# Kernel tuning notes

Measured on AMD Instinct MI355X. Metric: run time of the kernel, lower is better.

## Reference

```python
import jax, jax.numpy as jnp
import numpy as np

EPS_BN = 1e-5
EPS_NORM = 1e-12
NUM_HEADS = 8


def _bn_relu(x):
    # BatchNorm2d in training mode with fresh params (gamma=1, beta=0), then ReLU.
    m = x.mean((0, 2, 3), keepdims=True)
    v = x.var((0, 2, 3), keepdims=True)  # biased variance, as PyTorch uses for normalization
    return jax.nn.relu((x - m) * jax.lax.rsqrt(v + EPS_BN))


def _conv3(x, w, groups=1):
    # 3x3 conv, stride 1, padding 1 (NCHW / OIHW)
    return jax.lax.conv_general_dilated(
        x, w, (1, 1), ((1, 1), (1, 1)),
        dimension_numbers=('NCHW', 'OIHW', 'NCHW'),
        feature_group_count=groups)


def _encoder(x, w1, w2, w3):
    # Conv1x1 -> BN -> ReLU -> Conv k2 s2 -> BN -> ReLU -> Conv1x1 -> BN -> ReLU
    x = _bn_relu(jnp.einsum('bihw,oi->bohw', x, w1))
    b, c, h, w = x.shape
    # k=2,s=2 conv as a reshape + einsum (non-overlapping 2x2 patches)
    x = _bn_relu(jnp.einsum('bchpwq,ocpq->bohw', x.reshape(b, c, h // 2, 2, w // 2, 2), w2))
    return _bn_relu(jnp.einsum('bihw,oi->bohw', x, w3))


def _decoder(x, w1, w2, w3):
    # ConvT1x1 -> BN -> ReLU -> ConvT k2 s2 -> BN -> ReLU -> ConvT1x1 -> BN -> ReLU
    x = _bn_relu(jnp.einsum('bihw,io->bohw', x, w1))
    # ConvTranspose k=2,s=2: each input pixel expands to a 2x2 block
    y = jnp.einsum('bihw,iopq->bohpwq', x, w2)
    b, o, h, p, w, q = y.shape
    x = _bn_relu(y.reshape(b, o, h * p, w * q))
    return _bn_relu(jnp.einsum('bihw,io->bohw', x, w3))


def _l2norm(x):
    # F.normalize(dim=-1) with eps=1e-12
    return x / jnp.maximum(jnp.linalg.norm(x, axis=-1, keepdims=True), EPS_NORM)


def setup_inputs() -> dict:
    key = jax.random.key(0)
    ks = jax.random.split(key, 13)
    B, C, H, W = 8, 256, 64, 64
    d = C // 4  # attention dim after self.divide

    def rn(k, shape, s=0.1):
        return jax.random.normal(k, shape, jnp.float32) * s

    return {
        'x': jax.random.normal(ks[0], (B, C, H, W), jnp.float32),
        'y': jax.random.normal(ks[1], (B, C, H, W), jnp.float32),
        'temperature': jnp.ones((NUM_HEADS, 1, 1), jnp.float32),
        'enc_w1': rn(ks[2], (d // 2, C)),
        'enc_w2': rn(ks[3], (d // 2, d // 2, 2, 2)),
        'enc_w3': rn(ks[4], (d, d // 2)),
        'kv_w': rn(ks[5], (2 * d, d)),
        'kv_dw_w': rn(ks[6], (2 * d, 1, 3, 3)),
        'q_w': rn(ks[7], (d, d)),
        'q_dw_w': rn(ks[8], (d, d, 3, 3)),
        'proj_w': rn(ks[9], (d, d)),
        'dec_w1': rn(ks[10], (d, 2 * d)),
        'dec_w2': rn(ks[11], (2 * d, 2 * d, 2, 2)),
        'dec_w3': rn(ks[12], (2 * d, 4 * d)),
    }


def reference(x, y, temperature, enc_w1, enc_w2, enc_w3, kv_w, kv_dw_w,
              q_w, q_dw_w, proj_w, dec_w1, dec_w2, dec_w3):
    # Shared freshly-built encoder applied to both x and y (same weights,
    # BN batch stats computed per call).
    x = _encoder(x, enc_w1, enc_w2, enc_w3)
    y = _encoder(y, enc_w1, enc_w2, enc_w3)
    b, c, h, w = x.shape  # c = 64, h = w = 32

    kv = _conv3(jnp.einsum('bihw,oi->bohw', x, kv_w), kv_dw_w, groups=2 * c)
    k, v = jnp.split(kv, 2, axis=1)
    q = _conv3(jnp.einsum('bihw,oi->bohw', y, q_w), q_dw_w)  # regular 3x3 conv

    ch = c // NUM_HEADS
    heads = lambda t: t.reshape(b, NUM_HEADS, ch, h * w)  # b head c (h w)
    q, k, v = heads(q), heads(k), heads(v)
    q = _l2norm(q)
    k = _l2norm(k)
    temp = temperature[None]  # [1, head, 1, 1]

    # Spatial attention: [b, head, hw, hw]
    attn_s = jax.nn.softmax(jnp.einsum('bhcn,bhcm->bhnm', q, k) * temp, axis=-1)
    out_s = jnp.einsum('bhcn,bhnm->bhcm', v, attn_s).reshape(b, c, h, w)
    out_s = jnp.einsum('bihw,oi->bohw', out_s, proj_w)

    # Channel attention: [b, head, c, c]
    attn_c = jax.nn.softmax(jnp.einsum('bhcn,bhdn->bhcd', q, k) * temp, axis=-1)
    out_c = jnp.einsum('bhcd,bhdn->bhcn', attn_c, v).reshape(b, c, h, w)
    out_c = jnp.einsum('bihw,oi->bohw', out_c, proj_w)

    return _decoder(out_s + out_c, dec_w1, dec_w2, dec_w3)
```

## Files before the change

### kernel.cpp

```cpp
#include <hip/hip_runtime.h>
#include <hip/hip_bf16.h>

#define EPS_BN 1e-5f

template<int OT, bool HASBN, bool HASSTATS>
__global__ __launch_bounds__(256) void conv1x1_kernel(
    const float* __restrict__ in0, const float* __restrict__ in1,
    const float* __restrict__ w, float* __restrict__ out,
    const float* __restrict__ stIn, float* __restrict__ stOut,
    int I, int O, int P, int wio, int zsplit, float invN)
{
  __shared__ float wl[2048];
  __shared__ float bnm[256], bnr[256];
  int tid = threadIdx.x;
  int o0 = blockIdx.y*OT;
  int z  = blockIdx.z;
  int t  = (z >= zsplit) ? 1 : 0;
  int b  = t ? (z - zsplit) : z;
  const float* in = t ? in1 : in0;

  for(int idx=tid; idx<I*OT; idx+=256){
    int i = idx/OT, j = idx - i*OT;
    wl[idx] = wio ? w[(size_t)i*O + o0 + j] : w[(size_t)(o0+j)*I + i];
  }
  if(HASBN){
    for(int i=tid; i<I; i+=256){
      float s  = stIn[((size_t)t*I + i)*2];
      float s2 = stIn[((size_t)t*I + i)*2+1];
      float m  = s*invN;
      bnm[i] = m;
      bnr[i] = rsqrtf(s2*invN - m*m + EPS_BN);
    }
  }
  __syncthreads();

  int p4 = blockIdx.x*256 + tid;
  const float4* inb = (const float4*)(in + (size_t)b*I*P) + p4;
  int P4 = P >> 2;

  float acc[OT][4];
#pragma unroll
  for(int j=0;j<OT;j++){ acc[j][0]=acc[j][1]=acc[j][2]=acc[j][3]=0.f; }

  float4 vb[8];
  for(int i0=0;i0<I;i0+=8){
#pragma unroll
    for(int u=0;u<8;u++) vb[u] = inb[(size_t)(i0+u)*P4];
#pragma unroll
    for(int u=0;u<8;u++){
      float4 v = vb[u];
      if(HASBN){
        float m = bnm[i0+u], r = bnr[i0+u];
        v.x = fmaxf((v.x-m)*r, 0.f); v.y = fmaxf((v.y-m)*r, 0.f);
        v.z = fmaxf((v.z-m)*r, 0.f); v.w = fmaxf((v.w-m)*r, 0.f);
      }
      const float* wr = &wl[(i0+u)*OT];
#pragma unroll
      for(int j=0;j<OT;j++){
        float wv = wr[j];
        acc[j][0] = fmaf(wv, v.x, acc[j][0]);
        acc[j][1] = fmaf(wv, v.y, acc[j][1]);
        acc[j][2] = fmaf(wv, v.z, acc[j][2]);
        acc[j][3] = fmaf(wv, v.w, acc[j][3]);
      }
    }
  }

  float4* ob = (float4*)(out + ((size_t)z*O + o0)*P) + p4;
#pragma unroll
  for(int j=0;j<OT;j++){
    float4 vv = {acc[j][0], acc[j][1], acc[j][2], acc[j][3]};
    ob[(size_t)j*P4] = vv;
  }

  if(HASSTATS){
#pragma unroll
    for(int j=0;j<OT;j++){
      float s  = acc[j][0]+acc[j][1]+acc[j][2]+acc[j][3];
      float s2 = acc[j][0]*acc[j][0]+acc[j][1]*acc[j][1]
               + acc[j][2]*acc[j][2]+acc[j][3]*acc[j][3];
      for(int off=32; off>0; off>>=1){
        s  += __shfl_down(s,  off, 64);
        s2 += __shfl_down(s2, off, 64);
      }
      if((tid & 63)==0){
        atomicAdd(&stOut[((size_t)t*O + o0 + j)*2],   s);
        atomicAdd(&stOut[((size_t)t*O + o0 + j)*2+1], s2);
      }
    }
  }
}

template<int OT, bool HASBN, bool HASSTATS>
__global__ __launch_bounds__(256) void conv1x1_small(
    const float* __restrict__ in0, const float* __restrict__ in1,
    const float* __restrict__ w, float* __restrict__ out,
    const float* __restrict__ stIn, float* __restrict__ stOut,
    int I, int O, int wio, int zsplit, float invN)
{
  __shared__ float wl[512];
  __shared__ float bnm[128], bnr[128];
  int tid = threadIdx.x;
  int z  = blockIdx.z;
  int t  = (z >= zsplit) ? 1 : 0;
  int b  = t ? (z - zsplit) : z;
  const float* in = t ? in1 : in0;
  int W2 = 2*OT;

  for(int idx=tid; idx<I*W2; idx+=256){
    int i = idx/W2, slot = idx - i*W2;
    int oabs = blockIdx.y*W2 + slot;
    wl[idx] = wio ? w[(size_t)i*O + oabs] : w[(size_t)oabs*I + i];
  }
  if(HASBN){
    for(int i=tid; i<I; i+=256){
      float s  = stIn[((size_t)t*I + i)*2];
      float s2 = stIn[((size_t)t*I + i)*2+1];
      float m  = s*invN;
      bnm[i] = m;
      bnr[i] = rsqrtf(s2*invN - m*m + EPS_BN);
    }
  }
  __syncthreads();

  int p4 = blockIdx.x*128 + (tid & 127);
  int os = tid >> 7;
  const float4* inb = (const float4*)(in + (size_t)b*I*1024) + p4;

  float acc[OT][4];
#pragma unroll
  for(int j=0;j<OT;j++){ acc[j][0]=acc[j][1]=acc[j][2]=acc[j][3]=0.f; }

  float4 vb[8];
  for(int i0=0;i0<I;i0+=8){
#pragma unroll
    for(int u=0;u<8;u++) vb[u] = inb[(size_t)(i0+u)*256];
#pragma unroll
    for(int u=0;u<8;u++){
      float4 v = vb[u];
      if(HASBN){
        float m = bnm[i0+u], r = bnr[i0+u];
        v.x = fmaxf((v.x-m)*r, 0.f); v.y = fmaxf((v.y-m)*r, 0.f);
        v.z = fmaxf((v.z-m)*r, 0.f); v.w = fmaxf((v.w-m)*r, 0.f);
      }
      const float* wr = &wl[(i0+u)*W2 + os*OT];
#pragma unroll
      for(int j=0;j<OT;j++){
        float wv = wr[j];
        acc[j][0] = fmaf(wv, v.x, acc[j][0]);
        acc[j][1] = fmaf(wv, v.y, acc[j][1]);
        acc[j][2] = fmaf(wv, v.z, acc[j][2]);
        acc[j][3] = fmaf(wv, v.w, acc[j][3]);
      }
    }
  }

  int obase = blockIdx.y*W2 + os*OT;
  float4* ob = (float4*)(out + ((size_t)z*O + obase)*1024) + p4;
#pragma unroll
  for(int j=0;j<OT;j++){
    float4 vv = {acc[j][0], acc[j][1], acc[j][2], acc[j][3]};
    ob[(size_t)j*256] = vv;
  }

  if(HASSTATS){
#pragma unroll
    for(int j=0;j<OT;j++){
      float s  = acc[j][0]+acc[j][1]+acc[j][2]+acc[j][3];
      float s2 = acc[j][0]*acc[j][0]+acc[j][1]*acc[j][1]
               + acc[j][2]*acc[j][2]+acc[j][3]*acc[j][3];
      for(int off=32; off>0; off>>=1){
        s  += __shfl_down(s,  off, 64);
        s2 += __shfl_down(s2, off, 64);
      }
      if((tid & 63)==0){
        atomicAdd(&stOut[((size_t)t*O + obase + j)*2],   s);
        atomicAdd(&stOut[((size_t)t*O + obase + j)*2+1], s2);
      }
    }
  }
}

__global__ __launch_bounds__(256) void conv2x2s2_bn_kernel(
    const float* __restrict__ in, const float* __restrict__ w,
    float* __restrict__ out, const float* __restrict__ stIn,
    float* __restrict__ stOut, float invN)
{
  __shared__ float wl[512];
  __shared__ float bnm[32], bnr[32];
  int tid = threadIdx.x;
  int o0 = blockIdx.x*4;
  int rq = blockIdx.y;
  int z  = blockIdx.z;
  int t  = z >> 3;

  for(int idx=tid; idx<512; idx+=256){
    int osub = idx>>7, ch=(idx>>2)&31, pq=idx&3;
    wl[idx] = w[(((size_t)(o0+osub)*32 + ch)*4) + pq];
  }
  if(tid < 32){
    float s  = stIn[((size_t)t*32 + tid)*2];
    float s2 = stIn[((size_t)t*32 + tid)*2+1];
    float m  = s*invN;
    bnm[tid] = m;
    bnr[tid] = rsqrtf(s2*invN - m*m + EPS_BN);
  }
  __syncthreads();

  int os   = tid >> 6;
  int slot = tid & 63;
  int h    = rq*8 + (slot>>3);
  int wg   = slot & 7;
  int cb   = wg*8;
  const float* wbase = &wl[os*128];
  const float* inz = in + (size_t)z*32*4096;

  float acc[4] = {0,0,0,0};
  float4 c0,c1,c2,c3, n0_,n1_,n2_,n3_;
  c0 = *(const float4*)(inz + (size_t)0*4096 + (2*h)*64 + cb);
  c1 = *(const float4*)(inz + (size_t)0*4096 + (2*h)*64 + cb + 4);
  c2 = *(const float4*)(inz + (size_t)0*4096 + (2*h+1)*64 + cb);
  c3 = *(const float4*)(inz + (size_t)0*4096 + (2*h+1)*64 + cb + 4);
  for(int ch=0; ch<32; ch++){
    if(ch < 31){
      n0_ = *(const float4*)(inz + (size_t)(ch+1)*4096 + (2*h)*64 + cb);
      n1_ = *(const float4*)(inz + (size_t)(ch+1)*4096 + (2*h)*64 + cb + 4);
      n2_ = *(const float4*)(inz + (size_t)(ch+1)*4096 + (2*h+1)*64 + cb);
      n3_ = *(const float4*)(inz + (size_t)(ch+1)*4096 + (2*h+1)*64 + cb + 4);
    }
    float m = bnm[ch], r = bnr[ch];
    float t0[8] = {c0.x,c0.y,c0.z,c0.w,c1.x,c1.y,c1.z,c1.w};
    float t1[8] = {c2.x,c2.y,c2.z,c2.w,c3.x,c3.y,c3.z,c3.w};
#pragma unroll
    for(int e=0;e<8;e++){
      t0[e] = fmaxf((t0[e]-m)*r, 0.f);
      t1[e] = fmaxf((t1[e]-m)*r, 0.f);
    }
    const float* wp = wbase + ch*4;
#pragma unroll
    for(int k=0;k<4;k++){
      acc[k] = fmaf(wp[0], t0[2*k],   acc[k]);
      acc[k] = fmaf(wp[1], t0[2*k+1], acc[k]);
      acc[k] = fmaf(wp[2], t1[2*k],   acc[k]);
      acc[k] = fmaf(wp[3], t1[2*k+1], acc[k]);
    }
    c0=n0_; c1=n1_; c2=n2_; c3=n3_;
  }

  float4 vv = {acc[0],acc[1],acc[2],acc[3]};
  *(float4*)(out + ((size_t)z*32 + o0+os)*1024 + h*32 + wg*4) = vv;

  float s  = acc[0]+acc[1]+acc[2]+acc[3];
  float s2 = acc[0]*acc[0]+acc[1]*acc[1]+acc[2]*acc[2]+acc[3]*acc[3];
  for(int off=32; off>0; off>>=1){
    s  += __shfl_down(s,  off, 64);
    s2 += __shfl_down(s2, off, 64);
  }
  if((tid & 63)==0){
    atomicAdd(&stOut[((size_t)t*32 + o0 + os)*2],   s);
    atomicAdd(&stOut[((size_t)t*32 + o0 + os)*2+1], s2);
  }
}

__global__ __launch_bounds__(256) void upsample2x2_bn_kernel(
    const float* __restrict__ in, const float* __restrict__ w,
    float* __restrict__ out, const float* __restrict__ stIn,
    float* __restrict__ stOut, float invN)
{
  __shared__ float wl[1024];
  __shared__ float bnm[128], bnr[128];
  int tid = threadIdx.x;
  int o0 = blockIdx.x*2;
  int b  = blockIdx.y;

  for(int idx=tid; idx<1024; idx+=256){
    int pq = idx & 3, r = idx >> 2;
    int i = r >> 1, j = r & 1;
    wl[idx] = w[((size_t)i*128 + o0+j)*4 + pq];
  }
  if(tid < 128){
    float s  = stIn[(size_t)tid*2];
    float s2 = stIn[(size_t)tid*2+1];
    float m  = s*invN;
    bnm[tid] = m;
    bnr[tid] = rsqrtf(s2*invN - m*m + EPS_BN);
  }
  __syncthreads();

  int h  = tid >> 3;
  int wg = tid & 7;
  int w0 = wg*4;

  float acc[2][16];
#pragma unroll
  for(int j=0;j<2;j++) for(int e=0;e<16;e++) acc[j][e]=0.f;

  float4 vb4[8];
  for(int i0=0;i0<128;i0+=8){
#pragma unroll
    for(int u=0;u<8;u++)
      vb4[u] = *(const float4*)(in + (((size_t)b*128+i0+u)*1024) + h*32 + w0);
#pragma unroll
    for(int u=0;u<8;u++){
      int i = i0+u;
      float4 v = vb4[u];
      float m = bnm[i], r = bnr[i];
      float vk[4] = {fmaxf((v.x-m)*r,0.f), fmaxf((v.y-m)*r,0.f),
                     fmaxf((v.z-m)*r,0.f), fmaxf((v.w-m)*r,0.f)};
#pragma unroll
      for(int j=0;j<2;j++){
        const float* wj = &wl[(i*2+j)*4];
#pragma unroll
        for(int pq=0;pq<4;pq++){
#pragma unroll
          for(int k=0;k<4;k++)
            acc[j][pq*4+k] = fmaf(wj[pq], vk[k], acc[j][pq*4+k]);
        }
      }
    }
  }

#pragma unroll
  for(int j=0;j<2;j++){
    float* ob = out + ((size_t)b*128 + o0+j)*4096;
#pragma unroll
    for(int p=0;p<2;p++){
      float4 A = {acc[j][(p*2+0)*4+0], acc[j][(p*2+1)*4+0],
                  acc[j][(p*2+0)*4+1], acc[j][(p*2+1)*4+1]};
      float4 B = {acc[j][(p*2+0)*4+2], acc[j][(p*2+1)*4+2],
                  acc[j][(p*2+0)*4+3], acc[j][(p*2+1)*4+3]};
      *(float4*)(ob + (2*h+p)*64 + 2*w0)     = A;
      *(float4*)(ob + (2*h+p)*64 + 2*w0 + 4) = B;
    }
  }

#pragma unroll
  for(int j=0;j<2;j++){
    float s=0.f, s2=0.f;
#pragma unroll
    for(int e=0;e<16;e++){ s += acc[j][e]; s2 += acc[j][e]*acc[j][e]; }
    for(int off=32; off>0; off>>=1){
      s  += __shfl_down(s,  off, 64);
      s2 += __shfl_down(s2, off, 64);
    }
    if((tid & 63)==0){
      atomicAdd(&stOut[((size_t)(o0+j))*2],   s);
      atomicAdd(&stOut[((size_t)(o0+j))*2+1], s2);
    }
  }
}

__global__ __launch_bounds__(256) void bn_final_kernel(
    float* __restrict__ x, const float* __restrict__ st, float invN)
{
  int idx4 = blockIdx.x*256 + threadIdx.x;
  int c = (idx4 >> 10) & 255;
  float s  = st[(size_t)c*2];
  float s2 = st[(size_t)c*2+1];
  float m  = s*invN;
  float r  = rsqrtf(s2*invN - m*m + EPS_BN);
  float4 v = ((float4*)x)[idx4];
  v.x = fmaxf((v.x-m)*r, 0.f); v.y = fmaxf((v.y-m)*r, 0.f);
  v.z = fmaxf((v.z-m)*r, 0.f); v.w = fmaxf((v.w-m)*r, 0.f);
  ((float4*)x)[idx4] = v;
}

__global__ __launch_bounds__(256) void dwconv3x3_kernel(
    const float* __restrict__ in, const float* __restrict__ w,
    float* __restrict__ out, int C)
{
  int c = blockIdx.x, b = blockIdx.y;
  int tid = threadIdx.x;
  __shared__ float wl[9];
  if(tid < 9) wl[tid] = w[c*9 + tid];
  __syncthreads();
  int h = tid >> 3, x4 = tid & 7;
  int c0 = x4*4;
  const float* base = in + ((size_t)b*C + c)*1024;
  float ax=0.f, ay=0.f, az=0.f, aw=0.f;
#pragma unroll
  for(int dr=0; dr<3; dr++){
    int r = h + dr - 1;
    if((unsigned)r >= 32u) continue;
    const float* row = base + r*32 + c0;
    float4 cc = *(const float4*)row;
    float l  = (x4>0) ? row[-1] : 0.f;
    float rr = (x4<7) ? row[4]  : 0.f;
    float w0=wl[dr*3], w1=wl[dr*3+1], w2=wl[dr*3+2];
    ax = fmaf(w0,l,   fmaf(w1,cc.x, fmaf(w2,cc.y, ax)));
    ay = fmaf(w0,cc.x,fmaf(w1,cc.y, fmaf(w2,cc.z, ay)));
    az = fmaf(w0,cc.y,fmaf(w1,cc.z, fmaf(w2,cc.w, az)));
    aw = fmaf(w0,cc.z,fmaf(w1,cc.w, fmaf(w2,rr,  aw)));
  }
  float4 vv = {ax,ay,az,aw};
  *(float4*)(out + ((size_t)b*C + c)*1024 + h*32 + c0) = vv;
}

__global__ __launch_bounds__(256) void conv3x3_kernel(
    const float* __restrict__ in, const float* __restrict__ w,
    float* __restrict__ out, int IC)
{
  int o = blockIdx.x, b = blockIdx.y;
  int tid = threadIdx.x;
  __shared__ float wl[576];
  for(int t=tid; t<IC*9; t+=256) wl[t] = w[(size_t)o*IC*9 + t];
  __syncthreads();
  int h = tid >> 3, x4 = tid & 7;
  int c0 = x4*4;
  const float* inb = in + (size_t)b*IC*1024;
  float ax=0.f, ay=0.f, az=0.f, aw=0.f;
#pragma unroll 2
  for(int i=0;i<IC;i++){
    const float* base = inb + (size_t)i*1024;
    const float* wp = &wl[i*9];
#pragma unroll
    for(int dr=0; dr<3; dr++){
      int r = h + dr - 1;
      if((unsigned)r >= 32u) continue;
      const float* row = base + r*32 + c0;
      float4 cc = *(const float4*)row;
      float l  = (x4>0) ? row[-1] : 0.f;
      float rr = (x4<7) ? row[4]  : 0.f;
      float w0=wp[dr*3], w1=wp[dr*3+1], w2=wp[dr*3+2];
      ax = fmaf(w0,l,   fmaf(w1,cc.x, fmaf(w2,cc.y, ax)));
      ay = fmaf(w0,cc.x,fmaf(w1,cc.y, fmaf(w2,cc.z, ay)));
      az = fmaf(w0,cc.y,fmaf(w1,cc.z, fmaf(w2,cc.w, az)));
      aw = fmaf(w0,cc.z,fmaf(w1,cc.w, fmaf(w2,rr,  aw)));
    }
  }
  float4 vv = {ax,ay,az,aw};
  *(float4*)(out + ((size_t)b*gridDim.x + o)*1024 + h*32 + c0) = vv;
}

__global__ __launch_bounds__(256) void norm_scale_kernel(
    const float* __restrict__ q, const float* __restrict__ kv,
    float* __restrict__ scl)
{
  int r = blockIdx.x;
  const float* p;
  if(r < 512){ int b=r>>6, c=r&63; p = q + ((size_t)b*64+c)*1024; }
  else { int rr=r-512; int b=rr>>6, c=rr&63; p = kv + ((size_t)b*128+c)*1024; }
  int tid = threadIdx.x;
  float4 v = ((const float4*)p)[tid];
  float s = v.x*v.x + v.y*v.y + v.z*v.z + v.w*v.w;
  __shared__ float ls[256];
  ls[tid]=s; __syncthreads();
  for(int st=128; st>0; st>>=1){ if(tid<st) ls[tid]+=ls[tid+st]; __syncthreads(); }
  if(tid==0) scl[r] = 1.f/fmaxf(sqrtf(ls[0]), 1e-12f);
}

__global__ __launch_bounds__(256) void attn_pass1(
    const float* __restrict__ q, const float* __restrict__ kv,
    const float* __restrict__ temp, const float* __restrict__ scl,
    float* __restrict__ den_out)
{
  int bx = blockIdx.x, hh = blockIdx.y, b = blockIdx.z;
  int nchunk = bx >> 2, mq = bx & 3;
  int tid = threadIdx.x;
  __shared__ __align__(16) float kl[256*12];
  const float* kb = kv + ((size_t)b*128 + hh*8)*1024 + mq*256;
  for(int t=tid;t<2048;t+=256){
    int c=t>>8, m=t&255;
    kl[m*12+c] = kb[(size_t)c*1024+m] * scl[512 + b*64 + hh*8 + c];
  }
  __syncthreads();
  int n = nchunk*256 + tid;
  const float* qp = q + ((size_t)b*64 + hh*8)*1024 + n;
  float th = temp[hh];
  float mxb = fabsf(th);
  float qr[8];
#pragma unroll
  for(int c=0;c<8;c++) qr[c] = qp[(size_t)c*1024] * scl[b*64+hh*8+c] * th;
  const float4* kl4 = (const float4*)kl;
  float den = 0.f, den2 = 0.f;
  for(int m=0;m<256;m+=2){
    float4 a  = kl4[m*3],     a2 = kl4[m*3+1];
    float4 bt = kl4[(m+1)*3], b2 = kl4[(m+1)*3+1];
    float s0 = qr[0]*a.x+qr[1]*a.y+qr[2]*a.z+qr[3]*a.w
             + qr[4]*a2.x+qr[5]*a2.y+qr[6]*a2.z+qr[7]*a2.w;
    float s1 = qr[0]*bt.x+qr[1]*bt.y+qr[2]*bt.z+qr[3]*bt.w
             + qr[4]*b2.x+qr[5]*b2.y+qr[6]*b2.z+qr[7]*b2.w;
    den  += __expf(s0 - mxb);
    den2 += __expf(s1 - mxb);
  }
  atomicAdd(&den_out[((size_t)(b*8+hh))*1024+n], den+den2);
}

__global__ __launch_bounds__(256) void attn_pass2(
    const float* __restrict__ q, const float* __restrict__ kv,
    const float* __restrict__ temp, const float* __restrict__ scl,
    const float* __restrict__ den, float* __restrict__ out)
{
  int bx = blockIdx.x, hh = blockIdx.y, b = blockIdx.z;
  int mchunk = bx >> 2, nq = bx & 3;
  int tid = threadIdx.x;
  __shared__ __align__(16) float ql[256*12];
  __shared__ __align__(16) float vl[256*12];
  __shared__ float idl[256];
  int bh = b*8+hh;
  int n0 = nq*256;
  const float* qb = q  + ((size_t)b*64 + hh*8)*1024 + n0;
  const float* vb = kv + ((size_t)b*128 + 64 + hh*8)*1024 + n0;
  for(int t=tid;t<2048;t+=256){
    int c=t>>8, n=t&255;
    ql[n*12+c] = qb[(size_t)c*1024+n] * scl[b*64+hh*8+c];
    vl[n*12+c] = vb[(size_t)c*1024+n];
  }
  idl[tid] = 1.f/den[(size_t)bh*1024 + n0 + tid];
  __syncthreads();
  int m = mchunk*256 + tid;
  const float* kb = kv + ((size_t)b*128 + hh*8)*1024 + m;
  float th = temp[hh];
  float mxb = fabsf(th);
  float kr[8];
#pragma unroll
  for(int c=0;c<8;c++) kr[c] = kb[(size_t)c*1024] * scl[512+b*64+hh*8+c] * th;
  float acc[8] = {0,0,0,0,0,0,0,0};
  const float4* ql4 = (const float4*)ql;
  const float4* vl4 = (const float4*)vl;
  for(int n=0;n<256;n+=2){
    float4 qa = ql4[n*3],     qa2 = ql4[n*3+1];
    float4 qc = ql4[(n+1)*3], qc2 = ql4[(n+1)*3+1];
    float s0 = kr[0]*qa.x+kr[1]*qa.y+kr[2]*qa.z+kr[3]*qa.w
             + kr[4]*qa2.x+kr[5]*qa2.y+kr[6]*qa2.z+kr[7]*qa2.w;
    float s1 = kr[0]*qc.x+kr[1]*qc.y+kr[2]*qc.z+kr[3]*qc.w
             + kr[4]*qc2.x+kr[5]*qc2.y+kr[6]*qc2.z+kr[7]*qc2.w;
    float p0 = __expf(s0 - mxb) * idl[n];
    float p1 = __expf(s1 - mxb) * idl[n+1];
    float4 va = vl4[n*3],     va2 = vl4[n*3+1];
    float4 vc = vl4[(n+1)*3], vc2 = vl4[(n+1)*3+1];
    acc[0]+=p0*va.x + p1*vc.x; acc[1]+=p0*va.y + p1*vc.y;
    acc[2]+=p0*va.z + p1*vc.z; acc[3]+=p0*va.w + p1*vc.w;
    acc[4]+=p0*va2.x + p1*vc2.x; acc[5]+=p0*va2.y + p1*vc2.y;
    acc[6]+=p0*va2.z + p1*vc2.z; acc[7]+=p0*va2.w + p1*vc2.w;
  }
  float* ob = out + ((size_t)b*64 + hh*8)*1024 + m;
#pragma unroll
  for(int c=0;c<8;c++) atomicAdd(&ob[(size_t)c*1024], acc[c]);
}

__global__ __launch_bounds__(256) void attn_channel(
    const float* __restrict__ q, const float* __restrict__ kv,
    const float* __restrict__ temp, const float* __restrict__ scl,
    float* out)
{
  int hh = blockIdx.x, b = blockIdx.y;
  __shared__ float kl[8192];
  const float* qb = q  + ((size_t)b*64 + hh*8)*1024;
  const float* kb = kv + ((size_t)b*128 + hh*8)*1024;
  const float* vb = kv + ((size_t)b*128 + 64 + hh*8)*1024;
  int tid = threadIdx.x;
  for(int t=tid;t<8192;t+=256) kl[t]=kb[t];
  __syncthreads();
  __shared__ float part[256];
  __shared__ float a[64];
  {
    int pair = tid >> 2, seg = tid & 3;
    int c = pair >> 3, d = pair & 7;
    const float* qrow = qb + (size_t)c*1024 + seg*256;
    const float* krow = kl + d*1024 + seg*256;
    float s = 0.f;
#pragma unroll 4
    for(int n=0;n<256;n++) s += qrow[n]*krow[n];
    part[tid] = s;
  }
  __syncthreads();
  if(tid < 64){
    int c = tid >> 3, d = tid & 7;
    float g = part[tid*4]+part[tid*4+1]+part[tid*4+2]+part[tid*4+3];
    part[tid] = g * scl[b*64+hh*8+c] * scl[512+b*64+hh*8+d] * temp[hh];
  }
  __syncthreads();
  if(tid < 8){
    float mx = -3.4e38f;
    for(int d=0;d<8;d++) mx = fmaxf(mx, part[tid*8+d]);
    float den = 0.f;
    float e[8];
    for(int d=0;d<8;d++){ e[d] = __expf(part[tid*8+d]-mx); den+=e[d]; }
    float inv = 1.f/den;
    for(int d=0;d<8;d++) a[tid*8+d] = e[d]*inv;
  }
  __syncthreads();
  float* ob = out + ((size_t)b*64 + hh*8)*1024;
  for(int n=tid;n<1024;n+=256){
    float vv[8];
#pragma unroll
    for(int d=0;d<8;d++) vv[d] = vb[(size_t)d*1024+n];
#pragma unroll
    for(int c=0;c<8;c++){
      float s = 0.f;
#pragma unroll
      for(int d=0;d<8;d++) s += a[c*8+d]*vv[d];
      ob[(size_t)c*1024+n] += s;
    }
  }
}

extern "C" void kernel_launch(void* const* d_in, const int* in_sizes, int n_in,
                              void* d_out, int out_size, void* d_ws, size_t ws_size,
                              hipStream_t stream)
{
  (void)in_sizes; (void)n_in; (void)out_size; (void)ws_size;
  const float* x      = (const float*)d_in[0];
  const float* y      = (const float*)d_in[1];
  const float* temp   = (const float*)d_in[2];
  const float* enc_w1 = (const float*)d_in[3];
  const float* enc_w2 = (const float*)d_in[4];
  const float* enc_w3 = (const float*)d_in[5];
  const float* kv_w   = (const float*)d_in[6];
  const float* kv_dw_w= (const float*)d_in[7];
  const float* q_w    = (const float*)d_in[8];
  const float* q_dw_w = (const float*)d_in[9];
  const float* proj_w = (const float*)d_in[10];
  const float* dec_w1 = (const float*)d_in[11];
  const float* dec_w2 = (const float*)d_in[12];
  const float* dec_w3 = (const float*)d_in[13];
  float* out = (float*)d_out;

  float* W   = (float*)d_ws;
  float* ST  = W;
  float* ST0 = ST;
  float* ST1 = ST + 128;
  float* ST2 = ST + 256;
  float* ST3 = ST + 512;
  float* ST4 = ST + 768;
  float* ST5 = ST + 1024;
  float* A    = W + 2048;
  float* E1   = A;
  float* KV1  = A;
  float* QPre = A + 1048576;
  float* ATTN = A;
  float* PROJ = A + 524288;
  float* D1   = A + 1048576;
  float* E2   = W + 2099200;
  float* E3   = W + 2623488;
  float* KV   = W + 3672064;
  float* Q    = W + 4720640;
  float* SCL  = W + 5244928;
  float* DEN  = W + 5245952;
  float* D2   = W + 2099200;

  const float inv32k = 1.f/32768.f, inv8k = 1.f/8192.f;

  hipMemsetAsync(ST, 0, 2048*sizeof(float), stream);
  hipMemsetAsync(DEN, 0, 65536*sizeof(float), stream);

  conv1x1_kernel<4,false,true><<<dim3(4,8,16),256,0,stream>>>(
      x, y, enc_w1, E1, nullptr, ST0, 256, 32, 4096, 0, 8, 0.f);
  conv2x2s2_bn_kernel<<<dim3(8,4,16),256,0,stream>>>(E1, enc_w2, E2, ST0, ST1, inv32k);
  conv1x1_small<1,true,true><<<dim3(2,32,16),256,0,stream>>>(
      E2, E2 + (size_t)8*32*1024, enc_w3, E3, ST1, ST2, 32, 64, 0, 8, inv8k);

  conv1x1_small<1,true,false><<<dim3(2,64,8),256,0,stream>>>(
      E3, E3, kv_w, KV1, ST2, nullptr, 64, 128, 0, 999, inv8k);
  dwconv3x3_kernel<<<dim3(128,8),256,0,stream>>>(KV1, kv_dw_w, KV, 128);
  conv1x1_small<1,true,false><<<dim3(2,32,8),256,0,stream>>>(
      E3 + (size_t)8*64*1024, E3, q_w, QPre, ST2 + 128, nullptr, 64, 64, 0, 999, inv8k);
  conv3x3_kernel<<<dim3(64,8),256,0,stream>>>(QPre, q_dw_w, Q, 64);

  hipMemsetAsync(ATTN, 0, 524288*sizeof(float), stream);

  norm_scale_kernel<<<1024,256,0,stream>>>(Q, KV, SCL);

  attn_pass1<<<dim3(16,8,8),256,0,stream>>>(Q, KV, temp, SCL, DEN);
  attn_pass2<<<dim3(16,8,8),256,0,stream>>>(Q, KV, temp, SCL, DEN, ATTN);
  attn_channel<<<dim3(8,8),256,0,stream>>>(Q, KV, temp, SCL, ATTN);

  conv1x1_small<1,false,false><<<dim3(2,32,8),256,0,stream>>>(
      ATTN, ATTN, proj_w, PROJ, nullptr, nullptr, 64, 64, 0, 999, 0.f);

  conv1x1_small<1,false,true><<<dim3(2,64,8),256,0,stream>>>(
      PROJ, PROJ, dec_w1, D1, nullptr, ST3, 64, 128, 1, 999, 0.f);
  upsample2x2_bn_kernel<<<dim3(64,8),256,0,stream>>>(D1, dec_w2, D2, ST3, ST4, inv8k);
  conv1x1_kernel<8,true,true><<<dim3(4,32,8),256,0,stream>>>(
      D2, D2, dec_w3, out, ST4, ST5, 128, 256, 4096, 1, 999, inv32k);
  bn_final_kernel<<<8192,256,0,stream>>>(out, ST5, inv32k);
}
```

Before: 589.7 us.

## Stage 1x1 conv inputs in double-buffered LDS and raise output tiling

The large 1x1 conv kernel now stages an 8-channel input slab in double-buffered shared memory. That slab is shared by 4 wavefronts, and each wavefront computes a different group of output channels. Input is therefore read once per block for all outputs instead of once per output tile, and weights are read as float4. The small 1x1 convs get a larger per-thread output count with fewer blocks, and compiler memory fences are added to keep the loads grouped. The cost is higher register and LDS use and fewer blocks in the grid, which may reduce occupancy.

```diff
diff --git a/kernel.cpp b/kernel.cpp
--- a/kernel.cpp
+++ b/kernel.cpp
@@ -3,25 +3,40 @@
 
 #define EPS_BN 1e-5f
 
+#define PIPE_FENCE() asm volatile("" ::: "memory")
+
 template<int OT, bool HASBN, bool HASSTATS>
-__global__ __launch_bounds__(256) void conv1x1_kernel(
+__global__ __launch_bounds__(256,2) void conv1x1_lds(
     const float* __restrict__ in0, const float* __restrict__ in1,
     const float* __restrict__ w, float* __restrict__ out,
     const float* __restrict__ stIn, float* __restrict__ stOut,
     int I, int O, int P, int wio, int zsplit, float invN)
 {
-  __shared__ float wl[2048];
+  constexpr int OB = 4*OT;
+  __shared__ __align__(16) float wl[8192];
+  __shared__ __align__(16) float4 il[2][8][64];
   __shared__ float bnm[256], bnr[256];
-  int tid = threadIdx.x;
-  int o0 = blockIdx.y*OT;
-  int z  = blockIdx.z;
-  int t  = (z >= zsplit) ? 1 : 0;
-  int b  = t ? (z - zsplit) : z;
+
+  int tid = threadIdx.x;
+  int c   = tid & 63;
+  int g   = tid >> 6;
+  int z = blockIdx.z;
+  int t = (z >= zsplit) ? 1 : 0;
+  int b = t ? (z - zsplit) : z;
   const float* in = t ? in1 : in0;
-
-  for(int idx=tid; idx<I*OT; idx+=256){
-    int i = idx/OT, j = idx - i*OT;
-    wl[idx] = wio ? w[(size_t)i*O + o0 + j] : w[(size_t)(o0+j)*I + i];
+  int o0 = blockIdx.y*OB;
+  int P4 = P >> 2;
+
+  if(wio){
+    for(int idx=tid; idx<I*OB; idx+=256){
+      int i = idx/OB, oo = idx - i*OB;
+      wl[idx] = w[(size_t)i*O + o0 + oo];
+    }
+  } else {
+    for(int idx=tid; idx<I*OB; idx+=256){
+      int oo = idx/I, i = idx - oo*I;
+      wl[i*OB + oo] = w[(size_t)(o0+oo)*I + i];
+    }
   }
   if(HASBN){
     for(int i=tid; i<I; i+=256){
@@ -32,45 +47,65 @@
       bnr[i] = rsqrtf(s2*invN - m*m + EPS_BN);
     }
   }
-  __syncthreads();
-
-  int p4 = blockIdx.x*256 + tid;
-  const float4* inb = (const float4*)(in + (size_t)b*I*P) + p4;
-  int P4 = P >> 2;
+
+  const float4* inb = (const float4*)(in + (size_t)b*I*P) + (size_t)blockIdx.x*64;
+
+  float4 vr0 = inb[(size_t)g*P4 + c];
+  float4 vr1 = inb[(size_t)(g+4)*P4 + c];
+  il[0][g][c]   = vr0;
+  il[0][g+4][c] = vr1;
+  __syncthreads();
 
   float acc[OT][4];
 #pragma unroll
   for(int j=0;j<OT;j++){ acc[j][0]=acc[j][1]=acc[j][2]=acc[j][3]=0.f; }
 
-  float4 vb[8];
-  for(int i0=0;i0<I;i0+=8){
-#pragma unroll
-    for(int u=0;u<8;u++) vb[u] = inb[(size_t)(i0+u)*P4];
-#pragma unroll
-    for(int u=0;u<8;u++){
-      float4 v = vb[u];
+  int nchunk = I >> 3;
+  for(int k=0; k<nchunk; ++k){
+    int cur = k & 1;
+    if(k+1 < nchunk){
+      vr0 = inb[(size_t)((k+1)*8+g)*P4 + c];
+      vr1 = inb[(size_t)((k+1)*8+g+4)*P4 + c];
+    }
+    PIPE_FENCE();
+#pragma unroll
+    for(int ch=0; ch<8; ++ch){
+      float4 v = il[cur][ch][c];
       if(HASBN){
-        float m = bnm[i0+u], r = bnr[i0+u];
+        int i = k*8+ch;
+        float m = bnm[i], r = bnr[i];
         v.x = fmaxf((v.x-m)*r, 0.f); v.y = fmaxf((v.y-m)*r, 0.f);
         v.z = fmaxf((v.z-m)*r, 0.f); v.w = fmaxf((v.w-m)*r, 0.f);
       }
-      const float* wr = &wl[(i0+u)*OT];
-#pragma unroll
-      for(int j=0;j<OT;j++){
-        float wv = wr[j];
-        acc[j][0] = fmaf(wv, v.x, acc[j][0]);
-        acc[j][1] = fmaf(wv, v.y, acc[j][1]);
-        acc[j][2] = fmaf(wv, v.z, acc[j][2]);
-        acc[j][3] = fmaf(wv, v.w, acc[j][3]);
-      }
-    }
-  }
-
-  float4* ob = (float4*)(out + ((size_t)z*O + o0)*P) + p4;
+      const float4* wr4 = (const float4*)&wl[(k*8+ch)*OB + g*OT];
+#pragma unroll
+      for(int j4=0;j4<OT/4;j4++){
+        float4 wq = wr4[j4];
+        int j = j4*4;
+        acc[j  ][0]=fmaf(wq.x,v.x,acc[j  ][0]); acc[j  ][1]=fmaf(wq.x,v.y,acc[j  ][1]);
+        acc[j  ][2]=fmaf(wq.x,v.z,acc[j  ][2]); acc[j  ][3]=fmaf(wq.x,v.w,acc[j  ][3]);
+        acc[j+1][0]=fmaf(wq.y,v.x,acc[j+1][0]); acc[j+1][1]=fmaf(wq.y,v.y,acc[j+1][1]);
+        acc[j+1][2]=fmaf(wq.y,v.z,acc[j+1][2]); acc[j+1][3]=fmaf(wq.y,v.w,acc[j+1][3]);
+        acc[j+2][0]=fmaf(wq.z,v.x,acc[j+2][0]); acc[j+2][1]=fmaf(wq.z,v.y,acc[j+2][1]);
+        acc[j+2][2]=fmaf(wq.z,v.z,acc[j+2][2]); acc[j+2][3]=fmaf(wq.z,v.w,acc[j+2][3]);
+        acc[j+3][0]=fmaf(wq.w,v.x,acc[j+3][0]); acc[j+3][1]=fmaf(wq.w,v.y,acc[j+3][1]);
+        acc[j+3][2]=fmaf(wq.w,v.z,acc[j+3][2]); acc[j+3][3]=fmaf(wq.w,v.w,acc[j+3][3]);
+      }
+    }
+    PIPE_FENCE();
+    if(k+1 < nchunk){
+      int nxt = cur^1;
+      il[nxt][g][c]   = vr0;
+      il[nxt][g+4][c] = vr1;
+    }
+    __syncthreads();
+  }
+
+  float4* ob = (float4*)(out + (size_t)z*O*P) + (size_t)blockIdx.x*64 + c;
 #pragma unroll
   for(int j=0;j<OT;j++){
     float4 vv = {acc[j][0], acc[j][1], acc[j][2], acc[j][3]};
-    ob[(size_t)j*P4] = vv;
+    ob[(size_t)(o0 + g*OT + j)*P4] = vv;
   }
 
   if(HASSTATS){
@@ -84,8 +119,8 @@
         s2 += __shfl_down(s2, off, 64);
       }
       if((tid & 63)==0){
-        atomicAdd(&stOut[((size_t)t*O + o0 + j)*2],   s);
-        atomicAdd(&stOut[((size_t)t*O + o0 + j)*2+1], s2);
+        atomicAdd(&stOut[((size_t)t*O + o0 + g*OT + j)*2],   s);
+        atomicAdd(&stOut[((size_t)t*O + o0 + g*OT + j)*2+1], s2);
       }
     }
   }
@@ -135,6 +170,7 @@
   for(int i0=0;i0<I;i0+=8){
 #pragma unroll
     for(int u=0;u<8;u++) vb[u] = inb[(size_t)(i0+u)*256];
+    PIPE_FENCE();
 #pragma unroll
     for(int u=0;u<8;u++){
       float4 v = vb[u];
@@ -300,6 +336,7 @@
 #pragma unroll
     for(int u=0;u<8;u++)
       vb4[u] = *(const float4*)(in + (((size_t)b*128+i0+u)*1024) + h*32 + w0);
+    PIPE_FENCE();
 #pragma unroll
     for(int u=0;u<8;u++){
       int i = i0+u;
@@ -645,16 +682,16 @@
   hipMemsetAsync(ST, 0, 2048*sizeof(float), stream);
   hipMemsetAsync(DEN, 0, 65536*sizeof(float), stream);
 
-  conv1x1_kernel<4,false,true><<<dim3(4,8,16),256,0,stream>>>(
+  conv1x1_lds<8,false,true><<<dim3(16,1,16),256,0,stream>>>(
       x, y, enc_w1, E1, nullptr, ST0, 256, 32, 4096, 0, 8, 0.f);
   conv2x2s2_bn_kernel<<<dim3(8,4,16),256,0,stream>>>(E1, enc_w2, E2, ST0, ST1, inv32k);
-  conv1x1_small<1,true,true><<<dim3(2,32,16),256,0,stream>>>(
+  conv1x1_small<4,true,true><<<dim3(2,8,16),256,0,stream>>>(
       E2, E2 + (size_t)8*32*1024, enc_w3, E3, ST1, ST2, 32, 64, 0, 8, inv8k);
 
-  conv1x1_small<1,true,false><<<dim3(2,64,8),256,0,stream>>>(
+  conv1x1_small<4,true,false><<<dim3(2,16,8),256,0,stream>>>(
       E3, E3, kv_w, KV1, ST2, nullptr, 64, 128, 0, 999, inv8k);
   dwconv3x3_kernel<<<dim3(128,8),256,0,stream>>>(KV1, kv_dw_w, KV, 128);
-  conv1x1_small<1,true,false><<<dim3(2,32,8),256,0,stream>>>(
+  conv1x1_small<4,true,false><<<dim3(2,8,8),256,0,stream>>>(
       E3 + (size_t)8*64*1024, E3, q_w, QPre, ST2 + 128, nullptr, 64, 64, 0, 999, inv8k);
   conv3x3_kernel<<<dim3(64,8),256,0,stream>>>(QPre, q_dw_w, Q, 64);
 
@@ -666,13 +703,13 @@
   attn_pass2<<<dim3(16,8,8),256,0,stream>>>(Q, KV, temp, SCL, DEN, ATTN);
   attn_channel<<<dim3(8,8),256,0,stream>>>(Q, KV, temp, SCL, ATTN);
 
-  conv1x1_small<1,false,false><<<dim3(2,32,8),256,0,stream>>>(
+  conv1x1_small<4,false,false><<<dim3(2,8,8),256,0,stream>>>(
       ATTN, ATTN, proj_w, PROJ, nullptr, nullptr, 64, 64, 0, 999, 0.f);
 
-  conv1x1_small<1,false,true><<<dim3(2,64,8),256,0,stream>>>(
+  conv1x1_small<4,false,true><<<dim3(2,16,8),256,0,stream>>>(
       PROJ, PROJ, dec_w1, D1, nullptr, ST3, 64, 128, 1, 999, 0.f);
   upsample2x2_bn_kernel<<<dim3(64,8),256,0,stream>>>(D1, dec_w2, D2, ST3, ST4, inv8k);
-  conv1x1_kernel<8,true,true><<<dim3(4,32,8),256,0,stream>>>(
+  conv1x1_lds<16,true,true><<<dim3(16,4,8),256,0,stream>>>(
       D2, D2, dec_w3, out, ST4, ST5, 128, 256, 4096, 1, 999, inv32k);
   bn_final_kernel<<<8192,256,0,stream>>>(out, ST5, inv32k);
 }
```

Result: slower. 610.9 us (+3.6%).
